# Optimization experiments

Hardware: AMD Instinct MI355X
Metric: run time of the kernel (lower is better)

## Reference

```python
import jax, jax.numpy as jnp
import numpy as np

EPS = 1e-06


def setup_inputs() -> dict:
    key = jax.random.key(0)
    kq, kk, kv = jax.random.split(key, 3)
    B, H, L, DK, DV = 8, 8, 1024, 1024, 64  # code requires L == DK (see Z einsum)
    Q = jax.random.normal(kq, (B, H, L, DK), dtype=jnp.float32)
    K = jax.random.normal(kk, (B, H, L, DK), dtype=jnp.float32)
    V = jax.random.normal(kv, (B, H, L, DV), dtype=jnp.float32)
    return {"Q": Q, "K": K, "V": V}


def reference(Q, K, V):
    # Faithful translation of the torch module, with the einsums reduced to
    # their equivalent (and cheaper) elementwise/rowsum forms:
    #   KV  = einsum('bhlk,bhlv->bhlv', K', V)      == K'.sum(-1, keepdims) * V
    #   Zin = einsum('bhlk,bhl->bhl', Q', Ksum_k)   == Q'.sum(-1) * K'.sum(axis=2)
    #         (torch feeds K'.sum(dim=-2) of shape [b,h,k] into the 'bhl' slot,
    #          which is only valid because k == l here)
    #   out = einsum('bhlk,bhlv->bhlv', Q', KV) * Z == Q'.sum(-1)[...,None]*KV*Z
    Qp = jax.nn.elu(Q) + 1.0  # [b,h,l,k]
    Kp = jax.nn.elu(K) + 1.0  # [b,h,l,k]
    Kp_rowsum = Kp.sum(axis=-1)          # [b,h,l] (sum over k)
    KV = Kp_rowsum[..., None] * V        # [b,h,l,v]
    Qp_rowsum = Qp.sum(axis=-1)          # [b,h,l]
    Kp_colsum = Kp.sum(axis=2)           # [b,h,k] == [b,h,l] since k == l
    Z = 1.0 / (Qp_rowsum * Kp_colsum + EPS)  # [b,h,l]
    output = Qp_rowsum[..., None] * KV * Z[..., None]  # [b,h,l,v]
    return output
```

## Files before the change

### kernel.cpp

```cpp
#include <hip/hip_runtime.h>


#define EPS 1e-6f

constexpr int L   = 1024;
constexpr int DK  = 1024;
constexpr int DV  = 64;
constexpr int NBH = 64;
constexpr int RPB = 16;

__device__ __forceinline__ float elup(float x) {
    return x > 0.0f ? x + 1.0f : __expf(x);
}

__global__ __launch_bounds__(256, 8) void reduce_kernel(
    const float* __restrict__ Q, const float* __restrict__ K,
    float* __restrict__ colsum, float* __restrict__ rowsumQ,
    float* __restrict__ rowsumK)
{
    const int bh   = blockIdx.x / (L / RPB);
    const int rb   = blockIdx.x % (L / RPB);
    const int wave = threadIdx.x >> 6;
    const int lane = threadIdx.x & 63;

    const size_t tile_base = (size_t)bh * L * DK;

    float4 cacc[4];
    #pragma unroll
    for (int i = 0; i < 4; ++i) cacc[i] = make_float4(0.f, 0.f, 0.f, 0.f);

    for (int j = 0; j < RPB / 4; ++j) {
        const int row = rb * RPB + wave * (RPB / 4) + j;
        const float* qp = Q + tile_base + (size_t)row * DK + lane * 4;
        const float* kp = K + tile_base + (size_t)row * DK + lane * 4;

        float4 q[4], k[4];
        #pragma unroll
        for (int i = 0; i < 4; ++i) q[i] = *(const float4*)(qp + i * 256);
        #pragma unroll
        for (int i = 0; i < 4; ++i) k[i] = *(const float4*)(kp + i * 256);

        float rq = 0.f, rk = 0.f;
        #pragma unroll
        for (int i = 0; i < 4; ++i) {
            const float q0 = elup(q[i].x), q1 = elup(q[i].y);
            const float q2 = elup(q[i].z), q3 = elup(q[i].w);
            const float k0 = elup(k[i].x), k1 = elup(k[i].y);
            const float k2 = elup(k[i].z), k3 = elup(k[i].w);
            rq += (q0 + q1) + (q2 + q3);
            rk += (k0 + k1) + (k2 + k3);
            cacc[i].x += k0; cacc[i].y += k1; cacc[i].z += k2; cacc[i].w += k3;
        }

        #pragma unroll
        for (int m = 32; m >= 1; m >>= 1) {
            rq += __shfl_xor(rq, m, 64);
            rk += __shfl_xor(rk, m, 64);
        }
        if (lane == 0) {
            rowsumQ[bh * L + row] = rq;
            rowsumK[bh * L + row] = rk;
        }
    }

    __shared__ float scol[4 * DK];
    #pragma unroll
    for (int i = 0; i < 4; ++i) {
        *(float4*)&scol[wave * DK + i * 256 + lane * 4] = cacc[i];
    }
    __syncthreads();
    #pragma unroll
    for (int t = threadIdx.x; t < DK; t += 256) {
        const float s = scol[t] + scol[DK + t] + scol[2 * DK + t] + scol[3 * DK + t];
        atomicAdd(&colsum[bh * DK + t], s);
    }
}

__global__ __launch_bounds__(256) void finalize_kernel(
    const float* __restrict__ V, const float* __restrict__ colsum,
    const float* __restrict__ rowsumQ, const float* __restrict__ rowsumK,
    float* __restrict__ out)
{
    const int e4  = blockIdx.x * 256 + threadIdx.x;
    const int row = e4 >> 4;
    const float rq = rowsumQ[row];
    const float rk = rowsumK[row];
    const float cs = colsum[row];
    const float scale = rq * rk / (rq * cs + EPS);
    const float4 v = *(const float4*)(V + (size_t)e4 * 4);
    float4 o;
    o.x = v.x * scale; o.y = v.y * scale; o.z = v.z * scale; o.w = v.w * scale;
    *(float4*)(out + (size_t)e4 * 4) = o;
}

extern "C" void kernel_launch(void* const* d_in, const int* in_sizes, int n_in,
                              void* d_out, int out_size, void* d_ws, size_t ws_size,
                              hipStream_t stream) {
    const float* Q = (const float*)d_in[0];
    const float* K = (const float*)d_in[1];
    const float* V = (const float*)d_in[2];
    float* out = (float*)d_out;

    float* colsum  = (float*)d_ws;
    float* rowsumQ = colsum + NBH * L;
    float* rowsumK = rowsumQ + NBH * L;

    hipMemsetAsync(colsum, 0, (size_t)NBH * DK * sizeof(float), stream);

    reduce_kernel<<<NBH * (L / RPB), 256, 0, stream>>>(
        Q, K, colsum, rowsumQ, rowsumK);

    finalize_kernel<<<(NBH * L * DV / 4) / 256, 256, 0, stream>>>(
        V, colsum, rowsumQ, rowsumK, out);
}
```

Baseline: 542.1 us.

## Replace colsum atomics with per-block partials and a fold kernel

```diff
diff --git a/kernel.cpp b/kernel.cpp
--- a/kernel.cpp
+++ b/kernel.cpp
@@ -7,19 +7,21 @@
 constexpr int DK  = 1024;
 constexpr int DV  = 64;
 constexpr int NBH = 64;
-constexpr int RPB = 16;
+constexpr int RPB = 32;
+constexpr int NRB = L / RPB;
 
 __device__ __forceinline__ float elup(float x) {
     return x > 0.0f ? x + 1.0f : __expf(x);
 }
 
+template <bool ATOMIC>
 __global__ __launch_bounds__(256, 8) void reduce_kernel(
     const float* __restrict__ Q, const float* __restrict__ K,
-    float* __restrict__ colsum, float* __restrict__ rowsumQ,
+    float* __restrict__ colsum_or_partial, float* __restrict__ rowsumQ,
     float* __restrict__ rowsumK)
 {
-    const int bh   = blockIdx.x / (L / RPB);
-    const int rb   = blockIdx.x % (L / RPB);
+    const int bh   = blockIdx.x / NRB;
+    const int rb   = blockIdx.x % NRB;
     const int wave = threadIdx.x >> 6;
     const int lane = threadIdx.x & 63;
 
@@ -69,11 +71,37 @@
         *(float4*)&scol[wave * DK + i * 256 + lane * 4] = cacc[i];
     }
     __syncthreads();
-    #pragma unroll
-    for (int t = threadIdx.x; t < DK; t += 256) {
-        const float s = scol[t] + scol[DK + t] + scol[2 * DK + t] + scol[3 * DK + t];
-        atomicAdd(&colsum[bh * DK + t], s);
+    const float4* scol4 = (const float4*)scol;
+    const int t4 = threadIdx.x;
+    float4 a = scol4[t4], b = scol4[256 + t4];
+    float4 c = scol4[512 + t4], d = scol4[768 + t4];
+    float4 s;
+    s.x = (a.x + b.x) + (c.x + d.x);
+    s.y = (a.y + b.y) + (c.y + d.y);
+    s.z = (a.z + b.z) + (c.z + d.z);
+    s.w = (a.w + b.w) + (c.w + d.w);
+    if (ATOMIC) {
+        float* cs = colsum_or_partial + bh * DK + t4 * 4;
+        atomicAdd(cs + 0, s.x); atomicAdd(cs + 1, s.y);
+        atomicAdd(cs + 2, s.z); atomicAdd(cs + 3, s.w);
+    } else {
+        ((float4*)colsum_or_partial)[(size_t)blockIdx.x * 256 + t4] = s;
     }
+}
+
+__global__ __launch_bounds__(256) void colsum_fold_kernel(
+    const float* __restrict__ partial, float* __restrict__ colsum)
+{
+    const int bh = blockIdx.x;
+    const int t4 = threadIdx.x;
+    const float4* p4 = (const float4*)partial + (size_t)bh * NRB * 256 + t4;
+    float4 acc = make_float4(0.f, 0.f, 0.f, 0.f);
+    #pragma unroll 8
+    for (int rb = 0; rb < NRB; ++rb) {
+        const float4 v = p4[rb * 256];
+        acc.x += v.x; acc.y += v.y; acc.z += v.z; acc.w += v.w;
+    }
+    ((float4*)colsum)[bh * 256 + t4] = acc;
 }
 
 __global__ __launch_bounds__(256) void finalize_kernel(
@@ -104,11 +132,19 @@
     float* colsum  = (float*)d_ws;
     float* rowsumQ = colsum + NBH * L;
     float* rowsumK = rowsumQ + NBH * L;
+    float* partial = rowsumK + NBH * L;
 
-    hipMemsetAsync(colsum, 0, (size_t)NBH * DK * sizeof(float), stream);
+    const size_t need = (size_t)(3 * NBH * L + NBH * NRB * DK) * sizeof(float);
 
-    reduce_kernel<<<NBH * (L / RPB), 256, 0, stream>>>(
-        Q, K, colsum, rowsumQ, rowsumK);
+    if (ws_size >= need) {
+        reduce_kernel<false><<<NBH * NRB, 256, 0, stream>>>(
+            Q, K, partial, rowsumQ, rowsumK);
+        colsum_fold_kernel<<<NBH, 256, 0, stream>>>(partial, colsum);
+    } else {
+        hipMemsetAsync(colsum, 0, (size_t)NBH * DK * sizeof(float), stream);
+        reduce_kernel<true><<<NBH * NRB, 256, 0, stream>>>(
+            Q, K, colsum, rowsumQ, rowsumK);
+    }
 
     finalize_kernel<<<(NBH * L * DV / 4) / 256, 256, 0, stream>>>(
         V, colsum, rowsumQ, rowsumK, out);
```

Result: faster. 521.6 us (-3.8%).
